# Kernel tuning notes

Measured on AMD Instinct MI355X. Metric: run time of the kernel, lower is better.

## Reference

```python
import jax, jax.numpy as jnp
import numpy as np

NEG_INF = -1.0e9
LN_EPS = 1e-5
LEAK = 0.2


def setup_inputs() -> dict:
    key = jax.random.key(0)
    ks = jax.random.split(key, 8)
    B, C, T, N, H = 8, 64, 24, 512, 2
    hd = C // H
    x = jax.random.normal(ks[0], (B, C, T, N), dtype=jnp.float32)
    gso = jax.random.randint(ks[1], (N, N), 0, 2, dtype=jnp.int32)
    # torch nn.Linear weights are (out, in); xavier-ish scale
    s = (2.0 / (C + C)) ** 0.5
    Wq = jax.random.normal(ks[2], (C, C), dtype=jnp.float32) * s
    Wk = jax.random.normal(ks[3], (C, C), dtype=jnp.float32) * s
    Wv = jax.random.normal(ks[4], (C, C), dtype=jnp.float32) * s
    sa = (2.0 / (H + hd)) ** 0.5
    a_src = jax.random.normal(ks[5], (H, hd), dtype=jnp.float32) * sa
    a_dst = jax.random.normal(ks[6], (H, hd), dtype=jnp.float32) * sa
    ln_gamma = jnp.ones((C,), dtype=jnp.float32)
    ln_beta = jnp.zeros((C,), dtype=jnp.float32)
    return {"x": x, "gso": gso, "Wq": Wq, "Wk": Wk, "Wv": Wv,
            "a_src": a_src, "a_dst": a_dst, "ln_gamma": ln_gamma, "ln_beta": ln_beta}


def _spatial_gat(x, gso, Wq, Wk, Wv, a_src, a_dst, ln_gamma, ln_beta):
    B, C, T, N = x.shape
    H, hd = a_src.shape
    # (B, C, T, N) -> (B*T, N, C)
    xr = jnp.transpose(x, (0, 2, 3, 1)).reshape(B * T, N, C)
    # torch Linear: y = x @ W.T
    Q = jnp.einsum('bnc,dc->bnd', xr, Wq).reshape(B * T, N, H, hd)
    K = jnp.einsum('bnc,dc->bnd', xr, Wk).reshape(B * T, N, H, hd)
    V = jnp.einsum('bnc,dc->bnd', xr, Wv).reshape(B * T, N, H, hd)
    # additive GAT scores, all heads at once
    s_src = jnp.einsum('bnhd,hd->bnh', Q, a_src)  # (BT, N, H)
    s_dst = jnp.einsum('bnhd,hd->bnh', K, a_dst)  # (BT, N, H)
    scores = jax.nn.leaky_relu(s_src[:, :, None, :] + s_dst[:, None, :, :], LEAK)  # (BT, Ni, Nj, H)
    mask = jnp.where(gso == 0, jnp.float32(NEG_INF), jnp.float32(0.0))  # (N, N)
    scores = scores + mask[None, :, :, None]
    attn = jax.nn.softmax(scores, axis=2)  # softmax over destination j
    out = jnp.einsum('bijh,bjhd->bihd', attn, V)  # (BT, N, H, hd)
    out = out.reshape(B * T, N, C)
    # LayerNorm over channel dim
    mu = jnp.mean(out, axis=-1, keepdims=True)
    var = jnp.var(out, axis=-1, keepdims=True)
    out = (out - mu) * jax.lax.rsqrt(var + LN_EPS) * ln_gamma + ln_beta
    # back to (B, C, T, N)
    return jnp.transpose(out.reshape(B, T, N, C), (0, 3, 1, 2))


def reference(x, gso, Wq, Wk, Wv, a_src, a_dst, ln_gamma, ln_beta):
    return _spatial_gat(x, gso, Wq, Wk, Wv, a_src, a_dst, ln_gamma, ln_beta)
```

## Files before the change

### kernel.cpp

```cpp
#include <hip/hip_runtime.h>

#define CDIM 64
#define TDIM 24
#define NDIM 512
#define NBT  192

typedef float    float4v __attribute__((ext_vector_type(4)));
typedef _Float16 half8v  __attribute__((ext_vector_type(8)));
typedef _Float16 half4v  __attribute__((ext_vector_type(4)));
typedef _Float16 half2v  __attribute__((ext_vector_type(2)));


__device__ __forceinline__ float exp2_fast(float x) {
#if __has_builtin(__builtin_amdgcn_exp2f)
  return __builtin_amdgcn_exp2f(x);
#else
  return __expf(x * 0.69314718f);
#endif
}

__device__ __forceinline__ half2v pk2(float a, float b) {
  return __builtin_bit_cast(half2v, __builtin_amdgcn_cvt_pkrtz(a, b));
}

struct SmemK1 {
  union {
    _Float16 xt[128][72];
    _Float16 vtb[64][136];
  } big;
  _Float16 wv[64][72];
  _Float16 wext[16][72];
};

__launch_bounds__(256, 4)
__global__ void k1_v(const float* __restrict__ x,  const float* __restrict__ Wv,
                     const float* __restrict__ Wq, const float* __restrict__ Wk,
                     const float* __restrict__ a_src, const float* __restrict__ a_dst,
                     const int* __restrict__ gso,
                     _Float16* __restrict__ VT_g,
                     float* __restrict__ s_src_g, float* __restrict__ s_dst_g,
                     unsigned char* __restrict__ maskb) {
  const int t  = threadIdx.x;
  const int bx = blockIdx.x;

  if (bx >= 768) {
    int g = (bx - 768) * 256 + t;
    const int4* gp = (const int4*)gso + (size_t)g * 4;
    unsigned w[4];
#pragma unroll
    for (int k = 0; k < 4; ++k) {
      int4 v = gp[k];
      w[k] = (v.x ? 0x000000FFu : 0u) | (v.y ? 0x0000FF00u : 0u) |
             (v.z ? 0x00FF0000u : 0u) | (v.w ? 0xFF000000u : 0u);
    }
    uint4 o; o.x = w[0]; o.y = w[1]; o.z = w[2]; o.w = w[3];
    ((uint4*)maskb)[g] = o;
    return;
  }

  __shared__ SmemK1 sm;
  const int qn = bx & 3;
  const int bt = bx >> 2;
  const int b  = bt / TDIM, tt = bt % TDIM;
  const int n0 = qn * 128;

#pragma unroll
  for (int it = 0; it < 4; ++it) {
    int idx = it * 256 + t;
    int d = idx >> 4, k4 = (idx & 15) * 4;
    float4 v = ((const float4*)Wv)[idx];
    half2v p0 = pk2(v.x, v.y), p1 = pk2(v.z, v.w);
    half4v h4; h4[0] = p0[0]; h4[1] = p0[1]; h4[2] = p1[0]; h4[3] = p1[1];
    *(half4v*)&sm.wv[d][k4] = h4;
  }
  for (int z = t; z < 12 * 72; z += 256) ((_Float16*)sm.wext[4])[z] = (_Float16)0.f;
  {
    int r = t >> 6, c = t & 63;
    const float* av = (r & 2) ? a_dst : a_src;
    const float* W  = (r & 2) ? Wk : Wq;
    int off = (r & 1) * 32;
    float s = 0.f;
#pragma unroll
    for (int d = 0; d < 32; ++d)
      s += av[off + d] * W[(off + d) * 64 + c];
    sm.wext[r][c] = (_Float16)(s * 1.44269504f);
  }
  for (int it = 0; it < 16; ++it) {
    int idx = it * 256 + t;
    int cp = idx >> 7, n = idx & 127;
    int c0 = cp * 2;
    const float* base = x + ((size_t)(b * CDIM + c0) * TDIM + tt) * NDIM + n0 + n;
    *(half2v*)&sm.big.xt[n][c0] = pk2(base[0], base[(size_t)TDIM * NDIM]);
  }
  __syncthreads();

  const int lane = t & 63, w = t >> 6;
  const int m = lane & 15, quad = lane >> 4;
  const int mbase = w * 32;

  float4v acc[2][5];
#pragma unroll
  for (int mt = 0; mt < 2; ++mt)
#pragma unroll
    for (int nt = 0; nt < 5; ++nt)
#pragma unroll
      for (int r = 0; r < 4; ++r) acc[mt][nt][r] = 0.f;

#pragma unroll
  for (int ks = 0; ks < 2; ++ks) {
    half8v af[2], bf[5];
#pragma unroll
    for (int mt = 0; mt < 2; ++mt)
      af[mt] = *(const half8v*)&sm.big.xt[mbase + mt * 16 + m][ks * 32 + quad * 8];
#pragma unroll
    for (int nt = 0; nt < 4; ++nt)
      bf[nt] = *(const half8v*)&sm.wv[nt * 16 + m][ks * 32 + quad * 8];
    bf[4] = *(const half8v*)&sm.wext[m][ks * 32 + quad * 8];
#pragma unroll
    for (int mt = 0; mt < 2; ++mt)
#pragma unroll
      for (int nt = 0; nt < 5; ++nt)
        acc[mt][nt] = __builtin_amdgcn_mfma_f32_16x16x32_f16(af[mt], bf[nt], acc[mt][nt], 0, 0, 0);
  }

  if (m < 4) {
    float* basep = (m < 2 ? s_src_g : s_dst_g) + (size_t)(bt * 2 + (m & 1)) * NDIM;
#pragma unroll
    for (int mt = 0; mt < 2; ++mt)
#pragma unroll
      for (int r = 0; r < 4; ++r)
        basep[n0 + mbase + mt * 16 + quad * 4 + r] = acc[mt][4][r];
  }
  __syncthreads();

#pragma unroll
  for (int mt = 0; mt < 2; ++mt)
#pragma unroll
    for (int nt = 0; nt < 4; ++nt)
#pragma unroll
      for (int r = 0; r < 4; r += 2) {
        int nl = mbase + mt * 16 + quad * 4 + r;
        int c  = nt * 16 + m;
        *(half2v*)&sm.big.vtb[c][nl] = pk2(acc[mt][nt][r], acc[mt][nt][r + 1]);
      }
  __syncthreads();

  const unsigned* vdw = (const unsigned*)sm.big.vtb;
  unsigned* outdw = (unsigned*)VT_g;
  for (int it = 0; it < 16; ++it) {
    int idx = it * 256 + t;
    int c = idx >> 6, jd = idx & 63;
    outdw[(size_t)(bt * 64 + c) * 256 + qn * 64 + jd] = vdw[c * 68 + jd];
  }
}

struct SmemK2 {
  float otile[64][66];
  float rsum[4][64];
  float rsq[4][64];
  float mu[64], rs[64];
  _Float16 sF16[2][512];
  _Float16 sP16[2][512];
};

__launch_bounds__(256, 4)
__global__ void k2_attn(const _Float16* __restrict__ VT_g,
                        const float* __restrict__ s_src_g, const float* __restrict__ s_dst_g,
                        const unsigned char* __restrict__ maskb,
                        const float* __restrict__ gamma, const float* __restrict__ beta,
                        float* __restrict__ out) {
  __shared__ SmemK2 sm;
  const int t     = threadIdx.x;
  const int itile = blockIdx.x;
  const int bt    = blockIdx.y;
  const int i0    = itile * 64;
  const int b     = bt / TDIM, tt = bt % TDIM;
  const int lane  = t & 63, w = t >> 6;
  const int h = w >> 1, ihalf = w & 1;
  const int m = lane & 15, quad = lane >> 4;

  for (int it = 0; it < 4; ++it) {
    int idx = it * 256 + t;
    float d = s_dst_g[(size_t)bt * 2 * NDIM + idx];
    ((_Float16*)sm.sF16)[idx] = (_Float16)exp2_fast(d);
    ((_Float16*)sm.sP16)[idx] = (_Float16)exp2_fast(0.2f * d);
  }
  half8v E8[2], Q8[2];
#pragma unroll
  for (int mt = 0; mt < 2; ++mt) {
    float sv = s_src_g[(size_t)(bt * 2 + h) * NDIM + i0 + ihalf * 32 + mt * 16 + m];
    _Float16 ev = (_Float16)exp2_fast(sv - 6.f);
    _Float16 qv = (_Float16)exp2_fast(0.2f * sv - 6.f);
#pragma unroll
    for (int jj = 0; jj < 8; ++jj) { E8[mt][jj] = ev; Q8[mt][jj] = qv; }
  }

  float4v acc[2][2], accs[2];
#pragma unroll
  for (int mt = 0; mt < 2; ++mt) {
#pragma unroll
    for (int r = 0; r < 4; ++r) { acc[mt][0][r] = 0.f; acc[mt][1][r] = 0.f; accs[mt][r] = 0.f; }
  }
  const half8v bones = {(_Float16)1.f, (_Float16)1.f, (_Float16)1.f, (_Float16)1.f,
                        (_Float16)1.f, (_Float16)1.f, (_Float16)1.f, (_Float16)1.f};

  const _Float16* vrow = VT_g + ((size_t)bt * 64 + h * 32 + m) * NDIM;
  const unsigned char* mrow0 = maskb + (size_t)(i0 + ihalf * 32 + m) * NDIM;
  const unsigned char* mrow1 = mrow0 + 16 * NDIM;

  __syncthreads();

  for (int js = 0; js < 4; ++js) {
#pragma unroll
    for (int ksl = 0; ksl < 4; ++ksl) {
      int jo = js * 128 + ksl * 32 + quad * 8;
      half8v b0 = *(const half8v*)(vrow + jo);
      half8v b1 = *(const half8v*)(vrow + 16 * NDIM + jo);
      uint2 mv0 = *(const uint2*)(mrow0 + jo);
      uint2 mv1 = *(const uint2*)(mrow1 + jo);
      half8v F8 = *(const half8v*)&sm.sF16[h][jo];
      half8v P8 = *(const half8v*)&sm.sP16[h][jo];
#pragma unroll
      for (int mt = 0; mt < 2; ++mt) {
        uint2 mv = mt ? mv1 : mv0;
        half8v e8 = __builtin_elementwise_max(E8[mt] * F8, Q8[mt] * P8);
        uint4 eu = __builtin_bit_cast(uint4, e8);
        eu.x &= __builtin_amdgcn_perm(0u, mv.x, 0x01010000u);
        eu.y &= __builtin_amdgcn_perm(0u, mv.x, 0x03030202u);
        eu.z &= __builtin_amdgcn_perm(0u, mv.y, 0x01010000u);
        eu.w &= __builtin_amdgcn_perm(0u, mv.y, 0x03030202u);
        half8v af = __builtin_bit_cast(half8v, eu);
        acc[mt][0] = __builtin_amdgcn_mfma_f32_16x16x32_f16(af, b0,    acc[mt][0], 0, 0, 0);
        acc[mt][1] = __builtin_amdgcn_mfma_f32_16x16x32_f16(af, b1,    acc[mt][1], 0, 0, 0);
        accs[mt]   = __builtin_amdgcn_mfma_f32_16x16x32_f16(af, bones, accs[mt],   0, 0, 0);
      }
    }
  }

#pragma unroll
  for (int mt = 0; mt < 2; ++mt)
#pragma unroll
    for (int r = 0; r < 4; ++r) {
      float sc = __builtin_amdgcn_rcpf(accs[mt][r]);
      int i_loc = ihalf * 32 + mt * 16 + quad * 4 + r;
#pragma unroll
      for (int nt = 0; nt < 2; ++nt)
        sm.otile[i_loc][h * 32 + nt * 16 + m] = acc[mt][nt][r] * sc;
    }
  __syncthreads();

  {
    int i = t & 63, cg = t >> 6;
    float s1 = 0.f, s2 = 0.f;
#pragma unroll
    for (int cc = 0; cc < 16; ++cc) {
      float v = sm.otile[i][cg * 16 + cc];
      s1 += v; s2 += v * v;
    }
    sm.rsum[cg][i] = s1;
    sm.rsq[cg][i]  = s2;
  }
  __syncthreads();
  if (t < 64) {
    int i = t;
    float s1 = 0.f, s2 = 0.f;
#pragma unroll
    for (int cg = 0; cg < 4; ++cg) { s1 += sm.rsum[cg][i]; s2 += sm.rsq[cg][i]; }
    float mu  = s1 * (1.f / 64.f);
    float var = s2 * (1.f / 64.f) - mu * mu;
    sm.mu[i] = mu;
    sm.rs[i] = rsqrtf(var + 1e-5f);
  }
  __syncthreads();
  {
    int i = t & 63, cg = t >> 6;
    float mu = sm.mu[i], rs = sm.rs[i];
    int n = i0 + i;
#pragma unroll
    for (int cc = 0; cc < 16; ++cc) {
      int c = cg * 16 + cc;
      float v = (sm.otile[i][c] - mu) * rs * gamma[c] + beta[c];
      out[((size_t)(b * CDIM + c) * TDIM + tt) * NDIM + n] = v;
    }
  }
}

extern "C" void kernel_launch(void* const* d_in, const int* in_sizes, int n_in,
                              void* d_out, int out_size, void* d_ws, size_t ws_size,
                              hipStream_t stream) {
  const float* x     = (const float*)d_in[0];
  const int*   gso   = (const int*)d_in[1];
  const float* Wq    = (const float*)d_in[2];
  const float* Wk    = (const float*)d_in[3];
  const float* Wv    = (const float*)d_in[4];
  const float* a_src = (const float*)d_in[5];
  const float* a_dst = (const float*)d_in[6];
  const float* gamma = (const float*)d_in[7];
  const float* beta  = (const float*)d_in[8];
  float* out = (float*)d_out;

  char* ws = (char*)d_ws;
  _Float16* VT_g  = (_Float16*)ws;
  float*    s_src = (float*)(ws + 12582912);
  float*    s_dst = (float*)(ws + 13369344);
  unsigned char* maskb = (unsigned char*)(ws + 14155776);

  k1_v<<<832, 256, 0, stream>>>(x, Wv, Wq, Wk, a_src, a_dst, gso,
                                VT_g, s_src, s_dst, maskb);
  k2_attn<<<dim3(8, NBT), 256, 0, stream>>>(VT_g, s_src, s_dst, maskb, gamma, beta, out);
}
```

Measured before the change: 139.8 us.

## Stage V tiles in swizzled LDS, union smem, remap block order

The attention kernel now copies each 128-column slab of the transposed V into shared memory with an XOR swizzle and reads the MFMA B operands from there, instead of reading them straight from global memory. Shared buffers are overlapped with unions, which lets the occupancy hint rise from 4 to 6 blocks per SM. Both kernels switch to a 1D grid where consecutive blocks cover different bt values. The aim is coalesced V loads and better cache behaviour and occupancy, at the cost of extra barriers on every j-slab.

```diff
diff --git a/kernel.cpp b/kernel.cpp
--- a/kernel.cpp
+++ b/kernel.cpp
@@ -59,8 +59,8 @@
   }
 
   __shared__ SmemK1 sm;
-  const int qn = bx & 3;
-  const int bt = bx >> 2;
+  const int bt = bx % NBT;
+  const int qn = bx / NBT;
   const int b  = bt / TDIM, tt = bt % TDIM;
   const int n0 = qn * 128;
 
@@ -155,15 +155,17 @@
 }
 
 struct SmemK2 {
-  float otile[64][66];
-  float rsum[4][64];
-  float rsq[4][64];
-  float mu[64], rs[64];
-  _Float16 sF16[2][512];
-  _Float16 sP16[2][512];
+  union {
+    _Float16 vt[64][128];
+    float otile[64][66];
+  } u;
+  union {
+    struct { _Float16 F[2][512]; _Float16 P[2][512]; } f;
+    struct { float rsum[4][64]; float rsq[4][64]; float mu[64]; float rs[64]; } l;
+  } v;
 };
 
-__launch_bounds__(256, 4)
+__launch_bounds__(256, 6)
 __global__ void k2_attn(const _Float16* __restrict__ VT_g,
                         const float* __restrict__ s_src_g, const float* __restrict__ s_dst_g,
                         const unsigned char* __restrict__ maskb,
@@ -171,8 +173,9 @@
                         float* __restrict__ out) {
   __shared__ SmemK2 sm;
   const int t     = threadIdx.x;
-  const int itile = blockIdx.x;
-  const int bt    = blockIdx.y;
+  const int bx    = blockIdx.x;
+  const int bt    = bx % NBT;
+  const int itile = bx / NBT;
   const int i0    = itile * 64;
   const int b     = bt / TDIM, tt = bt % TDIM;
   const int lane  = t & 63, w = t >> 6;
@@ -182,8 +185,8 @@
   for (int it = 0; it < 4; ++it) {
     int idx = it * 256 + t;
     float d = s_dst_g[(size_t)bt * 2 * NDIM + idx];
-    ((_Float16*)sm.sF16)[idx] = (_Float16)exp2_fast(d);
-    ((_Float16*)sm.sP16)[idx] = (_Float16)exp2_fast(0.2f * d);
+    ((_Float16*)sm.v.f.F)[idx] = (_Float16)exp2_fast(d);
+    ((_Float16*)sm.v.f.P)[idx] = (_Float16)exp2_fast(0.2f * d);
   }
   half8v E8[2], Q8[2];
 #pragma unroll
@@ -204,22 +207,33 @@
   const half8v bones = {(_Float16)1.f, (_Float16)1.f, (_Float16)1.f, (_Float16)1.f,
                         (_Float16)1.f, (_Float16)1.f, (_Float16)1.f, (_Float16)1.f};
 
-  const _Float16* vrow = VT_g + ((size_t)bt * 64 + h * 32 + m) * NDIM;
   const unsigned char* mrow0 = maskb + (size_t)(i0 + ihalf * 32 + m) * NDIM;
   const unsigned char* mrow1 = mrow0 + 16 * NDIM;
-
-  __syncthreads();
+  const uint4* vsrc = (const uint4*)VT_g + (size_t)bt * 64 * 64;
+  const int r0 = h * 32 + m;
+  const int rsw = (r0 & 7) * 8;
 
   for (int js = 0; js < 4; ++js) {
+    __syncthreads();
+#pragma unroll
+    for (int it = 0; it < 4; ++it) {
+      int idx = it * 256 + t;
+      int c = idx >> 4, ch = idx & 15;
+      uint4 val = vsrc[c * 64 + js * 16 + ch];
+      *(uint4*)&sm.u.vt[c][(ch * 8) ^ ((c & 7) * 8)] = val;
+    }
+    __syncthreads();
+
 #pragma unroll
     for (int ksl = 0; ksl < 4; ++ksl) {
-      int jo = js * 128 + ksl * 32 + quad * 8;
-      half8v b0 = *(const half8v*)(vrow + jo);
-      half8v b1 = *(const half8v*)(vrow + 16 * NDIM + jo);
+      int jq = ksl * 32 + quad * 8;
+      int jo = js * 128 + jq;
+      half8v F8 = *(const half8v*)&sm.v.f.F[h][jo];
+      half8v P8 = *(const half8v*)&sm.v.f.P[h][jo];
+      half8v b0 = *(const half8v*)&sm.u.vt[r0][jq ^ rsw];
+      half8v b1 = *(const half8v*)&sm.u.vt[r0 + 16][jq ^ rsw];
       uint2 mv0 = *(const uint2*)(mrow0 + jo);
       uint2 mv1 = *(const uint2*)(mrow1 + jo);
-      half8v F8 = *(const half8v*)&sm.sF16[h][jo];
-      half8v P8 = *(const half8v*)&sm.sP16[h][jo];
 #pragma unroll
       for (int mt = 0; mt < 2; ++mt) {
         uint2 mv = mt ? mv1 : mv0;
@@ -237,6 +251,7 @@
     }
   }
 
+  __syncthreads();
 #pragma unroll
   for (int mt = 0; mt < 2; ++mt)
 #pragma unroll
@@ -245,7 +260,7 @@
       int i_loc = ihalf * 32 + mt * 16 + quad * 4 + r;
 #pragma unroll
       for (int nt = 0; nt < 2; ++nt)
-        sm.otile[i_loc][h * 32 + nt * 16 + m] = acc[mt][nt][r] * sc;
+        sm.u.otile[i_loc][h * 32 + nt * 16 + m] = acc[mt][nt][r] * sc;
     }
   __syncthreads();
 
@@ -254,32 +269,32 @@
     float s1 = 0.f, s2 = 0.f;
 #pragma unroll
     for (int cc = 0; cc < 16; ++cc) {
-      float v = sm.otile[i][cg * 16 + cc];
+      float v = sm.u.otile[i][cg * 16 + cc];
       s1 += v; s2 += v * v;
     }
-    sm.rsum[cg][i] = s1;
-    sm.rsq[cg][i]  = s2;
+    sm.v.l.rsum[cg][i] = s1;
+    sm.v.l.rsq[cg][i]  = s2;
   }
   __syncthreads();
   if (t < 64) {
     int i = t;
     float s1 = 0.f, s2 = 0.f;
 #pragma unroll
-    for (int cg = 0; cg < 4; ++cg) { s1 += sm.rsum[cg][i]; s2 += sm.rsq[cg][i]; }
+    for (int cg = 0; cg < 4; ++cg) { s1 += sm.v.l.rsum[cg][i]; s2 += sm.v.l.rsq[cg][i]; }
     float mu  = s1 * (1.f / 64.f);
     float var = s2 * (1.f / 64.f) - mu * mu;
-    sm.mu[i] = mu;
-    sm.rs[i] = rsqrtf(var + 1e-5f);
+    sm.v.l.mu[i] = mu;
+    sm.v.l.rs[i] = rsqrtf(var + 1e-5f);
   }
   __syncthreads();
   {
     int i = t & 63, cg = t >> 6;
-    float mu = sm.mu[i], rs = sm.rs[i];
+    float mu = sm.v.l.mu[i], rs = sm.v.l.rs[i];
     int n = i0 + i;
 #pragma unroll
     for (int cc = 0; cc < 16; ++cc) {
       int c = cg * 16 + cc;
-      float v = (sm.otile[i][c] - mu) * rs * gamma[c] + beta[c];
+      float v = (sm.u.otile[i][c] - mu) * rs * gamma[c] + beta[c];
       out[((size_t)(b * CDIM + c) * TDIM + tt) * NDIM + n] = v;
     }
   }
@@ -307,5 +322,5 @@
 
   k1_v<<<832, 256, 0, stream>>>(x, Wv, Wq, Wk, a_src, a_dst, gso,
                                 VT_g, s_src, s_dst, maskb);
-  k2_attn<<<dim3(8, NBT), 256, 0, stream>>>(VT_g, s_src, s_dst, maskb, gamma, beta, out);
-}
+  k2_attn<<<1536, 256, 0, stream>>>(VT_g, s_src, s_dst, maskb, gamma, beta, out);
+}
```

New measurement: 133.2 us. -4.7%, faster.
